# Performance work log

Measured on AMD Instinct MI355X. Metric: run time of the kernel, lower is better.

Reference implementation:

```python
import math
import jax, jax.numpy as jnp
import numpy as np

B, N, L, D, H = 1, 64, 512, 768, 12
DK = D // H


def setup_inputs() -> dict:
    rng = jax.random.key(0)
    ks = jax.random.split(rng, 8)
    s = 0.02  # weight init scale
    return {
        "query": jax.random.normal(ks[0], (B, N, L, D), jnp.float32),
        "key": jax.random.normal(ks[1], (B, N, L, D), jnp.float32),
        "value": jax.random.normal(ks[2], (B, N, L, D), jnp.float32),
        "Wq": jax.random.normal(ks[3], (D, D), jnp.float32) * s,
        "bq": jnp.zeros((D,), jnp.float32),
        "Wk": jax.random.normal(ks[4], (D, D), jnp.float32) * s,
        "bk": jnp.zeros((D,), jnp.float32),
        "Wv": jax.random.normal(ks[5], (D, D), jnp.float32) * s,
        "bv": jnp.zeros((D,), jnp.float32),
        "Wo": jax.random.normal(ks[6], (D, D), jnp.float32) * s,
        "bo": jnp.zeros((D,), jnp.float32),
    }


def reference(query, key, value, Wq, bq, Wk, bk, Wv, bv, Wo, bo):
    b, n, l, d = query.shape
    h, dk = H, DK
    # combined scaling: 1/sqrt(d_k) * 1/sqrt(N)
    scale = 1.0 / (math.sqrt(dk) * math.sqrt(n))
    # nn.Linear: y = x @ W.T + b  (W is [out, in])
    q = (jnp.einsum('bnld,ed->bnle', query, Wq) + bq).reshape(b, n, l, h, dk) * scale
    k = (jnp.einsum('bnld,ed->bnle', key, Wk) + bk).reshape(b, n, l, h, dk)
    v = (jnp.einsum('bnld,ed->bnle', value, Wv) + bv).reshape(b, n, l, h, dk)
    # tied attention: scores summed over the N (sequence-copy) axis BEFORE softmax
    att = jnp.einsum('bnihk,bnjhk->bhij', q, k)  # [B,H,L,L]
    att = jax.nn.softmax(att, axis=-1)  # dropout is identity in eval
    # single attention map broadcast across all N value tensors
    out = jnp.einsum('bhij,bnjhk->bnihk', att, v).reshape(b, n, l, d)
    return jnp.einsum('bnld,ed->bnle', out, Wo) + bo
```

## Files before the change

### kernel.cpp

```cpp
#include <hip/hip_runtime.h>


typedef __bf16 bf16x8 __attribute__((ext_vector_type(8)));
typedef float f32x4 __attribute__((ext_vector_type(4)));

__device__ __forceinline__ unsigned short f2bf(float f) {
  unsigned u = __float_as_uint(f);
  u += 0x7fffu + ((u >> 16) & 1u);
  return (unsigned short)(u >> 16);
}

__device__ __forceinline__ void gll16(const void* g, void* l) {
  __builtin_amdgcn_global_load_lds(
      (const __attribute__((address_space(1))) unsigned int*)g,
      (__attribute__((address_space(3))) unsigned int*)l, 16, 0, 0);
}

#define BAR __builtin_amdgcn_s_barrier()

enum { MODE_QCAT = 0, MODE_VT = 1, MODE_ATT = 2, MODE_OUTWS = 3, MODE_OUT_BIAS = 4 };

template <int MODE>
__global__ __launch_bounds__(512, 2) void gemm256(
    const void* __restrict__ Av, const void* __restrict__ Bv,
    const float* __restrict__ b0, const float* __restrict__ b1,
    void* __restrict__ Cv, int K, int lda, int ldb,
    long long a_bs, long long b_bs, float alpha0, float alpha1,
    long long c_bs, int ntn) {
  __shared__ unsigned short L[2][2][16384];

  const int tid = threadIdx.x;
  const int wave = tid >> 6;
  const int lane = tid & 63;
  const int wm = wave >> 2;
  const int wn = wave & 3;
  const int l15 = lane & 15;
  const int kq8 = lane >> 4;
  const int sw = l15 & 7;

  int tm, tn, batch, ks = 0;
  if constexpr (MODE == MODE_ATT) {
    tm = blockIdx.x >> 1;
    tn = blockIdx.x & 1;
    batch = blockIdx.z % 12;
    ks = blockIdx.z / 12;
  } else if constexpr (MODE == MODE_OUTWS) {
    tm = blockIdx.x >> 4;
    tn = blockIdx.x & 15;
    batch = blockIdx.z;
  } else {
    const int bid = blockIdx.x;
    const int xcd = bid & 7;
    const int kk_ = bid >> 3;
    tn = kk_ % ntn;
    tm = (kk_ / ntn) * 8 + xcd;
    batch = blockIdx.z;
  }

  const long long m0 = (long long)tm * 256;
  const long long n0 = (long long)tn * 256;

  const unsigned short* Ab = (const unsigned short*)Av + (long long)batch * a_bs +
                             (long long)ks * K;
  const unsigned short* Bb = (const unsigned short*)Bv + (long long)batch * b_bs +
                             (long long)ks * K;

  const long long rowAw = m0 + wave * 8 + (lane >> 3);
  const long long rowBw = n0 + wave * 8 + (lane >> 3);
  const int csw = ((lane & 7) ^ (lane >> 3)) << 3;

  f32x4 acc[8][4] = {};

  auto stA = [&](int buf, int q, int k0) {
    gll16(Ab + (rowAw + (q << 6)) * (long long)lda + k0 + csw,
          &L[buf][0][(q << 12) + (wave << 9)]);
  };
  auto stB = [&](int buf, int q, int k0) {
    gll16(Bb + (rowBw + (q << 6)) * (long long)ldb + k0 + csw,
          &L[buf][1][(q << 12) + (wave << 9)]);
  };

  float bpre[4] = {};
  float aa = 1.0f;
  if constexpr (MODE == MODE_QCAT || MODE == MODE_VT || MODE == MODE_OUT_BIAS) {
    const float* bb = batch ? b1 : b0;
    aa = batch ? alpha1 : alpha0;
#pragma unroll
    for (int u = 0; u < 4; ++u) bpre[u] = bb[n0 + wn * 64 + u * 16 + l15];
  }

  const int NT = K >> 6;
#pragma unroll
  for (int q = 0; q < 4; ++q) stB(0, q, 0);
#pragma unroll
  for (int q = 0; q < 4; ++q) stA(0, q, 0);
  if (NT > 1) {
    stA(1, 0, 64);
    stA(1, 2, 64);
    asm volatile("s_waitcnt vmcnt(2)" ::: "memory");
  } else {
    asm volatile("s_waitcnt vmcnt(0)" ::: "memory");
  }
  BAR;

  for (int T = 0; T < NT; ++T) {
    const int cur = T & 1, nxt = cur ^ 1;
    const int k1 = (T + 1) << 6, k2 = (T + 2) << 6;
#pragma unroll
    for (int p = 0; p < 4; ++p) {
      const int kc = p >> 1, mh = p & 1;
      bf16x8 af[4], bfr[4];
#pragma unroll
      for (int mf = 0; mf < 4; ++mf) {
        const int row = wm * 128 + mh * 64 + mf * 16 + l15;
        af[mf] = *(const bf16x8*)&L[cur][0][row * 64 + (((kc << 2) + kq8) ^ sw) * 8];
      }
#pragma unroll
      for (int u = 0; u < 4; ++u) {
        const int row = wn * 64 + u * 16 + l15;
        bfr[u] = *(const bf16x8*)&L[cur][1][row * 64 + (((kc << 2) + kq8) ^ sw) * 8];
      }
      if (p == 0 && T + 1 < NT) { stB(nxt, 0, k1); stB(nxt, 1, k1); }
      if (p == 1 && T + 1 < NT) { stB(nxt, 2, k1); stB(nxt, 3, k1); }
      if (p == 2 && T + 1 < NT) { stA(nxt, 1, k1); stA(nxt, 3, k1); }
      if (p == 3 && T + 2 < NT) { stA(cur, 0, k2); stA(cur, 2, k2); }
      __builtin_amdgcn_s_setprio(1);
#pragma unroll
      for (int mf = 0; mf < 4; ++mf)
#pragma unroll
        for (int u = 0; u < 4; ++u)
          acc[mh * 4 + mf][u] = __builtin_amdgcn_mfma_f32_16x16x32_bf16(
              af[mf], bfr[u], acc[mh * 4 + mf][u], 0, 0, 0);
      __builtin_amdgcn_s_setprio(0);
      if (p == 3) {
        if (T + 1 < NT) {
          if (T + 2 < NT) asm volatile("s_waitcnt vmcnt(2)" ::: "memory");
          else            asm volatile("s_waitcnt vmcnt(0)" ::: "memory");
          BAR;
        }
      } else {
        BAR;
      }
    }
  }

#pragma unroll
  for (int mf = 0; mf < 8; ++mf) {
#pragma unroll
    for (int u = 0; u < 4; ++u) {
      const long long col = n0 + wn * 64 + u * 16 + l15;
#pragma unroll
      for (int r = 0; r < 4; ++r) {
        const long long row = m0 + wm * 128 + mf * 16 + (lane >> 4) * 4 + r;
        float v = acc[mf][u][r];
        if constexpr (MODE == MODE_QCAT) {
          const float vv = (v + bpre[u]) * aa;
          const long long h = col >> 6, kq = col & 63, n = row >> 9, i = row & 511;
          ((unsigned short*)Cv + batch * c_bs)[((h * 512 + i) << 12) + (n << 6) + kq] =
              f2bf(vv);
        } else if constexpr (MODE == MODE_VT) {
          const float vv = v + bpre[u];
          const long long h = col >> 6, kq = col & 63, n = row >> 9, j = row & 511;
          ((unsigned short*)Cv)[(((h << 12) + (n << 6) + kq) << 9) + j] = f2bf(vv);
        } else if constexpr (MODE == MODE_ATT) {
          ((float*)Cv)[((long long)(ks * 12 + batch) << 18) + (row << 9) + col] = v;
        } else if constexpr (MODE == MODE_OUTWS) {
          const long long n = col >> 6, kk = col & 63;
          ((unsigned short*)Cv)[(n * 512 + row) * 768 + (long long)batch * 64 + kk] =
              f2bf(v);
        } else {
          ((float*)Cv)[row * 768 + col] = v + bpre[u];
        }
      }
    }
  }
}

__global__ __launch_bounds__(256) void softmax_rows(const float* __restrict__ att,
                                                    unsigned short* __restrict__ outb) {
  const long long rowbase = (long long)blockIdx.x << 9;
  const int tid = threadIdx.x;
  float a = 0.0f, b = 0.0f;
#pragma unroll
  for (int s = 0; s < 8; ++s) {
    a += att[(long long)s * 3145728 + rowbase + tid];
    b += att[(long long)s * 3145728 + rowbase + tid + 256];
  }

  float m = fmaxf(a, b);
#pragma unroll
  for (int off = 32; off; off >>= 1) m = fmaxf(m, __shfl_down(m, off));
  __shared__ float redm[4];
  if ((tid & 63) == 0) redm[tid >> 6] = m;
  __syncthreads();
  m = fmaxf(fmaxf(redm[0], redm[1]), fmaxf(redm[2], redm[3]));

  const float e0 = __expf(a - m), e1 = __expf(b - m);
  float s = e0 + e1;
#pragma unroll
  for (int off = 32; off; off >>= 1) s += __shfl_down(s, off);
  __shared__ float reds[4];
  if ((tid & 63) == 0) reds[tid >> 6] = s;
  __syncthreads();
  s = reds[0] + reds[1] + reds[2] + reds[3];

  const float inv = 1.0f / s;
  outb[rowbase + tid] = f2bf(e0 * inv);
  outb[rowbase + tid + 256] = f2bf(e1 * inv);
}

__global__ __launch_bounds__(256) void cvt_bf16(const float* __restrict__ in,
                                                unsigned short* __restrict__ out) {
  const long long i = ((long long)blockIdx.x * 256 + threadIdx.x) * 8;
  const float4 a = *(const float4*)(in + i);
  const float4 b = *(const float4*)(in + i + 4);
  uint4 p;
  p.x = (unsigned)f2bf(a.x) | ((unsigned)f2bf(a.y) << 16);
  p.y = (unsigned)f2bf(a.z) | ((unsigned)f2bf(a.w) << 16);
  p.z = (unsigned)f2bf(b.x) | ((unsigned)f2bf(b.y) << 16);
  p.w = (unsigned)f2bf(b.z) | ((unsigned)f2bf(b.w) << 16);
  *(uint4*)(out + i) = p;
}

__global__ __launch_bounds__(256) void cvt_qk(
    const float* __restrict__ s0, const float* __restrict__ s1,
    unsigned short* __restrict__ d0, unsigned short* __restrict__ d1) {
  const float* s = blockIdx.y ? s1 : s0;
  unsigned short* d = blockIdx.y ? d1 : d0;
  const long long i = ((long long)blockIdx.x * 256 + threadIdx.x) * 8;
  const float4 a = *(const float4*)(s + i);
  const float4 b = *(const float4*)(s + i + 4);
  uint4 p;
  p.x = (unsigned)f2bf(a.x) | ((unsigned)f2bf(a.y) << 16);
  p.y = (unsigned)f2bf(a.z) | ((unsigned)f2bf(a.w) << 16);
  p.z = (unsigned)f2bf(b.x) | ((unsigned)f2bf(b.y) << 16);
  p.w = (unsigned)f2bf(b.z) | ((unsigned)f2bf(b.w) << 16);
  *(uint4*)(d + i) = p;
}

__global__ __launch_bounds__(256) void cvt_w4(
    const float* __restrict__ s0, const float* __restrict__ s1,
    const float* __restrict__ s2, const float* __restrict__ s3,
    unsigned short* __restrict__ d0, unsigned short* __restrict__ d1,
    unsigned short* __restrict__ d2, unsigned short* __restrict__ d3) {
  const float* s;
  unsigned short* d;
  switch (blockIdx.y) {
    case 0: s = s0; d = d0; break;
    case 1: s = s1; d = d1; break;
    case 2: s = s2; d = d2; break;
    default: s = s3; d = d3; break;
  }
  const long long i = ((long long)blockIdx.x * 256 + threadIdx.x) * 8;
  const float4 a = *(const float4*)(s + i);
  const float4 b = *(const float4*)(s + i + 4);
  uint4 p;
  p.x = (unsigned)f2bf(a.x) | ((unsigned)f2bf(a.y) << 16);
  p.y = (unsigned)f2bf(a.z) | ((unsigned)f2bf(a.w) << 16);
  p.z = (unsigned)f2bf(b.x) | ((unsigned)f2bf(b.y) << 16);
  p.w = (unsigned)f2bf(b.z) | ((unsigned)f2bf(b.w) << 16);
  *(uint4*)(d + i) = p;
}

extern "C" void kernel_launch(void* const* d_in, const int* in_sizes, int n_in,
                              void* d_out, int out_size, void* d_ws, size_t ws_size,
                              hipStream_t stream) {
  const float* query = (const float*)d_in[0];
  const float* key   = (const float*)d_in[1];
  const float* value = (const float*)d_in[2];
  const float* Wq = (const float*)d_in[3];
  const float* bq = (const float*)d_in[4];
  const float* Wk = (const float*)d_in[5];
  const float* bk = (const float*)d_in[6];
  const float* Wv = (const float*)d_in[7];
  const float* bv = (const float*)d_in[8];
  const float* Wo = (const float*)d_in[9];
  const float* bo = (const float*)d_in[10];
  float* out = (float*)d_out;

  char* ws = (char*)d_ws;
  unsigned short* q_ws  = (unsigned short*)(ws);
  unsigned short* k_ws  = (unsigned short*)(ws + 50331648);
  unsigned short* vt_ws = (unsigned short*)(ws + 100663296);
  unsigned short* wq_b  = (unsigned short*)(ws + 150994944);
  unsigned short* wk_b  = (unsigned short*)(ws + 150994944 + 1179648);
  unsigned short* wv_b  = (unsigned short*)(ws + 150994944 + 2359296);
  unsigned short* wo_b  = (unsigned short*)(ws + 150994944 + 3538944);
  unsigned short* att_b = k_ws;
  unsigned short* out_ws = q_ws;
  unsigned short* xb0 = (unsigned short*)d_out;
  unsigned short* xb1 = (unsigned short*)d_out + 25165824;
  float* att_part = (float*)d_out;

  const dim3 blk(256);
  const dim3 blk5(512);

  cvt_w4<<<dim3(288, 4), blk, 0, stream>>>(Wq, Wk, Wv, Wo, wq_b, wk_b, wv_b, wo_b);

  cvt_qk<<<dim3(12288, 2), blk, 0, stream>>>(query, key, xb0, xb1);

  gemm256<MODE_QCAT><<<dim3(384, 1, 2), blk5, 0, stream>>>(
      xb0, wq_b, bq, bk, q_ws, 768, 768, 768, 25165824LL, 589824LL,
      0.015625f, 1.0f, 25165824LL, 3);

  cvt_bf16<<<12288, blk, 0, stream>>>(value, xb0);
  gemm256<MODE_VT><<<dim3(384, 1, 1), blk5, 0, stream>>>(
      xb0, wv_b, bv, nullptr, vt_ws, 768, 768, 768, 0, 0, 1.0f, 1.0f, 0, 3);

  gemm256<MODE_ATT><<<dim3(4, 1, 96), blk5, 0, stream>>>(
      q_ws, k_ws, nullptr, nullptr, att_part, 512, 4096, 4096,
      2097152LL, 2097152LL, 1.0f, 1.0f, 0, 0);

  softmax_rows<<<6144, blk, 0, stream>>>(att_part, att_b);

  gemm256<MODE_OUTWS><<<dim3(32, 1, 12), blk5, 0, stream>>>(
      att_b, vt_ws, nullptr, nullptr, out_ws, 512, 512, 512,
      262144LL, 2097152LL, 1.0f, 1.0f, 0, 0);

  gemm256<MODE_OUT_BIAS><<<dim3(384, 1, 1), blk5, 0, stream>>>(
      out_ws, wo_b, bo, nullptr, out, 768, 768, 768, 0, 0, 1.0f, 1.0f, 0, 3);
}
```

Baseline: 633.6 us.

## Merge all bf16 conversions into one kernel and halve attention split-K partials

Replaces the three conversion kernels with one cvt_all launch that converts query, key, value and all four weights, using nontemporal 16-float-per-thread loads. Value is now converted into the k workspace and its projection runs before the Q/K projection, so the separate value conversion pass goes away. The attention score GEMM now uses 4 split-K slices of length 1024 instead of 8 of 512, and softmax sums only 4 partials, which cuts partial-buffer traffic but halves the grid size. The partial buffer moves to the second half of the output buffer. This relies on the value-derived data in the k workspace being consumed before the Q/K projection overwrites it.

```diff
diff --git a/kernel.cpp b/kernel.cpp
--- a/kernel.cpp
+++ b/kernel.cpp
@@ -182,7 +182,7 @@
   const int tid = threadIdx.x;
   float a = 0.0f, b = 0.0f;
 #pragma unroll
-  for (int s = 0; s < 8; ++s) {
+  for (int s = 0; s < 4; ++s) {
     a += att[(long long)s * 3145728 + rowbase + tid];
     b += att[(long long)s * 3145728 + rowbase + tid + 256];
   }
@@ -209,57 +209,43 @@
   outb[rowbase + tid + 256] = f2bf(e1 * inv);
 }
 
-__global__ __launch_bounds__(256) void cvt_bf16(const float* __restrict__ in,
-                                                unsigned short* __restrict__ out) {
-  const long long i = ((long long)blockIdx.x * 256 + threadIdx.x) * 8;
-  const float4 a = *(const float4*)(in + i);
-  const float4 b = *(const float4*)(in + i + 4);
-  uint4 p;
-  p.x = (unsigned)f2bf(a.x) | ((unsigned)f2bf(a.y) << 16);
-  p.y = (unsigned)f2bf(a.z) | ((unsigned)f2bf(a.w) << 16);
-  p.z = (unsigned)f2bf(b.x) | ((unsigned)f2bf(b.y) << 16);
-  p.w = (unsigned)f2bf(b.z) | ((unsigned)f2bf(b.w) << 16);
-  *(uint4*)(out + i) = p;
-}
-
-__global__ __launch_bounds__(256) void cvt_qk(
-    const float* __restrict__ s0, const float* __restrict__ s1,
-    unsigned short* __restrict__ d0, unsigned short* __restrict__ d1) {
-  const float* s = blockIdx.y ? s1 : s0;
-  unsigned short* d = blockIdx.y ? d1 : d0;
-  const long long i = ((long long)blockIdx.x * 256 + threadIdx.x) * 8;
-  const float4 a = *(const float4*)(s + i);
-  const float4 b = *(const float4*)(s + i + 4);
-  uint4 p;
-  p.x = (unsigned)f2bf(a.x) | ((unsigned)f2bf(a.y) << 16);
-  p.y = (unsigned)f2bf(a.z) | ((unsigned)f2bf(a.w) << 16);
-  p.z = (unsigned)f2bf(b.x) | ((unsigned)f2bf(b.y) << 16);
-  p.w = (unsigned)f2bf(b.z) | ((unsigned)f2bf(b.w) << 16);
-  *(uint4*)(d + i) = p;
-}
-
-__global__ __launch_bounds__(256) void cvt_w4(
-    const float* __restrict__ s0, const float* __restrict__ s1,
-    const float* __restrict__ s2, const float* __restrict__ s3,
-    unsigned short* __restrict__ d0, unsigned short* __restrict__ d1,
-    unsigned short* __restrict__ d2, unsigned short* __restrict__ d3) {
+__global__ __launch_bounds__(256) void cvt_all(
+    const float* __restrict__ q, const float* __restrict__ k,
+    const float* __restrict__ v, const float* __restrict__ wq,
+    const float* __restrict__ wk, const float* __restrict__ wv,
+    const float* __restrict__ wo, unsigned short* __restrict__ dq,
+    unsigned short* __restrict__ dk, unsigned short* __restrict__ dv,
+    unsigned short* __restrict__ dwq, unsigned short* __restrict__ dwk,
+    unsigned short* __restrict__ dwv, unsigned short* __restrict__ dwo) {
+  const int b = blockIdx.x;
   const float* s;
   unsigned short* d;
-  switch (blockIdx.y) {
-    case 0: s = s0; d = d0; break;
-    case 1: s = s1; d = d1; break;
-    case 2: s = s2; d = d2; break;
-    default: s = s3; d = d3; break;
-  }
-  const long long i = ((long long)blockIdx.x * 256 + threadIdx.x) * 8;
-  const float4 a = *(const float4*)(s + i);
-  const float4 b = *(const float4*)(s + i + 4);
-  uint4 p;
-  p.x = (unsigned)f2bf(a.x) | ((unsigned)f2bf(a.y) << 16);
-  p.y = (unsigned)f2bf(a.z) | ((unsigned)f2bf(a.w) << 16);
-  p.z = (unsigned)f2bf(b.x) | ((unsigned)f2bf(b.y) << 16);
-  p.w = (unsigned)f2bf(b.z) | ((unsigned)f2bf(b.w) << 16);
-  *(uint4*)(d + i) = p;
+  long long blk;
+  if (b < 1536) { s = q; d = dq; blk = b; }
+  else if (b < 3072) { s = k; d = dk; blk = b - 1536; }
+  else if (b < 4608) { s = v; d = dv; blk = b - 3072; }
+  else {
+    const int w = b - 4608;
+    const int t = w / 36;
+    blk = w % 36;
+    s = t == 0 ? wq : (t == 1 ? wk : (t == 2 ? wv : wo));
+    d = t == 0 ? dwq : (t == 1 ? dwk : (t == 2 ? dwv : dwo));
+  }
+  const long long base = blk * 16384;
+  const int tid = threadIdx.x;
+
+  f32x4 r[16];
+#pragma unroll
+  for (int c = 0; c < 16; ++c)
+    r[c] = __builtin_nontemporal_load(
+        (const f32x4*)(s + base + (long long)(c * 256 + tid) * 4));
+#pragma unroll
+  for (int c = 0; c < 16; ++c) {
+    uint2 p;
+    p.x = (unsigned)f2bf(r[c][0]) | ((unsigned)f2bf(r[c][1]) << 16);
+    p.y = (unsigned)f2bf(r[c][2]) | ((unsigned)f2bf(r[c][3]) << 16);
+    *(uint2*)(d + base + (long long)(c * 256 + tid) * 4) = p;
+  }
 }
 
 extern "C" void kernel_launch(void* const* d_in, const int* in_sizes, int n_in,
@@ -290,25 +276,24 @@
   unsigned short* out_ws = q_ws;
   unsigned short* xb0 = (unsigned short*)d_out;
   unsigned short* xb1 = (unsigned short*)d_out + 25165824;
-  float* att_part = (float*)d_out;
+  unsigned short* xbv = k_ws;
+  float* att_part = (float*)((char*)d_out + 50331648);
 
   const dim3 blk(256);
   const dim3 blk5(512);
 
-  cvt_w4<<<dim3(288, 4), blk, 0, stream>>>(Wq, Wk, Wv, Wo, wq_b, wk_b, wv_b, wo_b);
-
-  cvt_qk<<<dim3(12288, 2), blk, 0, stream>>>(query, key, xb0, xb1);
+  cvt_all<<<4752, blk, 0, stream>>>(query, key, value, Wq, Wk, Wv, Wo,
+                                    xb0, xb1, xbv, wq_b, wk_b, wv_b, wo_b);
+
+  gemm256<MODE_VT><<<dim3(384, 1, 1), blk5, 0, stream>>>(
+      xbv, wv_b, bv, nullptr, vt_ws, 768, 768, 768, 0, 0, 1.0f, 1.0f, 0, 3);
 
   gemm256<MODE_QCAT><<<dim3(384, 1, 2), blk5, 0, stream>>>(
       xb0, wq_b, bq, bk, q_ws, 768, 768, 768, 25165824LL, 589824LL,
       0.015625f, 1.0f, 25165824LL, 3);
 
-  cvt_bf16<<<12288, blk, 0, stream>>>(value, xb0);
-  gemm256<MODE_VT><<<dim3(384, 1, 1), blk5, 0, stream>>>(
-      xb0, wv_b, bv, nullptr, vt_ws, 768, 768, 768, 0, 0, 1.0f, 1.0f, 0, 3);
-
-  gemm256<MODE_ATT><<<dim3(4, 1, 96), blk5, 0, stream>>>(
-      q_ws, k_ws, nullptr, nullptr, att_part, 512, 4096, 4096,
+  gemm256<MODE_ATT><<<dim3(4, 1, 48), blk5, 0, stream>>>(
+      q_ws, k_ws, nullptr, nullptr, att_part, 1024, 4096, 4096,
       2097152LL, 2097152LL, 1.0f, 1.0f, 0, 0);
 
   softmax_rows<<<6144, blk, 0, stream>>>(att_part, att_b);
```

Result: faster. 583.2 us (-8.0%).
